# Kernel tuning notes

Hardware: AMD Instinct MI355X
Metric: run time of the kernel (lower is better)

Reference implementation:

```python
import jax, jax.numpy as jnp
import numpy as np

B, S, D = 2, 8192, 1024
H, HD, FD = 16, 64, 256

def setup_inputs() -> dict:
    key = jax.random.key(0)
    ks = jax.random.split(key, 6)
    sc = 1.0 / np.sqrt(D)
    return {
        "hidden_states": jax.random.normal(ks[0], (B, S, D), jnp.float32),
        "Wq": jax.random.normal(ks[1], (D, D), jnp.float32) * sc,
        "Wk": jax.random.normal(ks[2], (D, D), jnp.float32) * sc,
        "Wv": jax.random.normal(ks[3], (D, D), jnp.float32) * sc,
        "Wo": jax.random.normal(ks[4], (D, D), jnp.float32) * sc,
        "Wf": jax.random.normal(ks[5], (FD, HD), jnp.float32) * (1.0 / np.sqrt(HD)),
    }

def reference(hidden_states, Wq, Wk, Wv, Wo, Wf):
    b, s, _ = hidden_states.shape
    # projections (torch Linear: x @ W.T), split heads -> (b, s, h, hd)
    q = (hidden_states @ Wq.T).reshape(b, s, H, HD)
    k = (hidden_states @ Wk.T).reshape(b, s, H, HD)
    v = (hidden_states @ Wv.T).reshape(b, s, H, HD)
    # elu+1 feature map -> (b, s, h, f)
    qf = jax.nn.elu(q @ Wf.T) + 1.0
    kf = jax.nn.elu(k @ Wf.T) + 1.0
    # global kv summary: (b, h, f, d)
    kv = jnp.einsum('bshf,bshd->bhfd', kf, v)
    out = jnp.einsum('bshf,bhfd->bshd', qf, kv)
    k_sum = kf.sum(axis=1)                       # (b, h, f)
    norm = jnp.einsum('bshf,bhf->bsh', qf, k_sum)[..., None] + 1e-6
    out = (out / norm).reshape(b, s, D)
    return out @ Wo.T
```

## Files before the change

kernel.cpp:

```cpp
#include <hip/hip_runtime.h>
#include <stdint.h>

typedef __bf16 bf16_t;
typedef __attribute__((ext_vector_type(8))) __bf16 bfv8;
typedef __attribute__((ext_vector_type(4))) __bf16 bfv4;
typedef __attribute__((ext_vector_type(4))) float f32x4;

constexpr int BATCH = 2, SEQ = 8192, DIM = 1024, NH = 16, HDIM = 64, FDIM = 256;
constexpr int MROWS = BATCH * SEQ;
constexpr int NCHUNK = 16;
constexpr int KV_NIT = (SEQ / NCHUNK) / 32;
constexpr int KVP_CH = 32 * 256 * 68;

__device__ __forceinline__ f32x4 mfma_bf16(bfv8 a, bfv8 b, f32x4 c) {
  return __builtin_amdgcn_mfma_f32_16x16x32_bf16(a, b, c, 0, 0, 0);
}

__device__ __forceinline__ void gload_lds16(const bf16_t* g, bf16_t* lds) {
  auto const* gp = reinterpret_cast<const __attribute__((address_space(1))) uint32_t*>(
      reinterpret_cast<uintptr_t>(g));
  auto* lp = reinterpret_cast<__attribute__((address_space(3))) uint32_t*>(
      reinterpret_cast<uintptr_t>(lds));
  __builtin_amdgcn_global_load_lds(gp, lp, 16, 0, 0);
}

__device__ __forceinline__ void stage128x64(const bf16_t* g_base, int k0,
                                            bf16_t* lds, int wid, int lane) {
#pragma unroll
  for (int j = 0; j < 4; ++j) {
    int r0 = (wid * 4 + j) * 8;
    int g_row = r0 + (lane >> 3);
    int g_slot = (lane & 7) ^ (g_row & 7);
    const bf16_t* src = g_base + (size_t)g_row * DIM + k0 + g_slot * 8;
    gload_lds16(src, lds + r0 * 64);
  }
}

__global__ __launch_bounds__(256) void cvt_all(const float* __restrict__ X,
                                               const float* __restrict__ Wq,
                                               const float* __restrict__ Wk,
                                               const float* __restrict__ Wv,
                                               const float* __restrict__ Wo,
                                               const float* __restrict__ Wf,
                                               bf16_t* __restrict__ Xb,
                                               bf16_t* __restrict__ W3,
                                               bf16_t* __restrict__ Wob,
                                               bf16_t* __restrict__ Wfb) {
  int i = blockIdx.x * 256 + threadIdx.x;
  const float* src;
  bf16_t* dst;
  int off;
  if (i < 4194304) {
    src = X; dst = Xb; off = i;
  } else {
    int j = i - 4194304;
    if (j < 786432) {
      int seg = j >> 18;
      off = j & 262143;
      src = (seg == 0) ? Wq : ((seg == 1) ? Wk : Wv);
      dst = W3 + (size_t)seg * 1048576;
    } else if (j < 1048576) {
      off = j - 786432; src = Wo; dst = Wob;
    } else {
      off = j - 1048576; src = Wf; dst = Wfb;
    }
  }
  float4 v = reinterpret_cast<const float4*>(src)[off];
  bfv4 o = {(__bf16)v.x, (__bf16)v.y, (__bf16)v.z, (__bf16)v.w};
  reinterpret_cast<bfv4*>(dst)[off] = o;
}

__global__ __launch_bounds__(256) void gemm_qkv(const bf16_t* __restrict__ A,
                                                const bf16_t* __restrict__ Wall,
                                                bf16_t* __restrict__ Q,
                                                bf16_t* __restrict__ K,
                                                bf16_t* __restrict__ V) {
  __shared__ bf16_t As[2][128 * 64];
  __shared__ bf16_t Bs[2][128 * 64];
  int z = blockIdx.z;
  const bf16_t* Wm = Wall + (size_t)z * (DIM * DIM);
  bf16_t* C = (z == 0) ? Q : ((z == 1) ? K : V);
  int lane = threadIdx.x & 63, wid = threadIdx.x >> 6;
  int lr = lane & 15, lg = lane >> 4;
  int wr = wid >> 1, wc = wid & 1;
  int brow = blockIdx.x * 128, bcol = blockIdx.y * 128;
  const bf16_t* Ab = A + (size_t)brow * DIM;
  const bf16_t* Bb = Wm + (size_t)bcol * DIM;
  f32x4 acc[4][4] = {};

  stage128x64(Ab, 0, As[0], wid, lane);
  stage128x64(Bb, 0, Bs[0], wid, lane);
  asm volatile("s_waitcnt vmcnt(0)" ::: "memory");
  __builtin_amdgcn_s_barrier();

  auto TILE = [&](const bf16_t* Acur, const bf16_t* Bcur, bf16_t* Anext, bf16_t* Bnext,
                  int knext) __attribute__((always_inline)) {
    if (knext < DIM) {
      stage128x64(Ab, knext, Anext, wid, lane);
      stage128x64(Bb, knext, Bnext, wid, lane);
    }
#pragma unroll
    for (int kk = 0; kk < 2; ++kk) {
      bfv8 af[4], bg[4];
#pragma unroll
      for (int t = 0; t < 4; ++t) {
        int ar = wr * 64 + t * 16 + lr;
        af[t] = *reinterpret_cast<const bfv8*>(&Acur[ar * 64 + (((kk * 4 + lg) ^ (ar & 7)) * 8)]);
        int br = wc * 64 + t * 16 + lr;
        bg[t] = *reinterpret_cast<const bfv8*>(&Bcur[br * 64 + (((kk * 4 + lg) ^ (br & 7)) * 8)]);
      }
#pragma unroll
      for (int i = 0; i < 4; ++i)
#pragma unroll
        for (int j = 0; j < 4; ++j) acc[i][j] = mfma_bf16(af[i], bg[j], acc[i][j]);
    }
    asm volatile("s_waitcnt vmcnt(0)" ::: "memory");
    __builtin_amdgcn_s_barrier();
  };

  for (int ks = 0; ks < DIM / 64; ks += 2) {
    TILE(As[0], Bs[0], As[1], Bs[1], (ks + 1) * 64);
    TILE(As[1], Bs[1], As[0], Bs[0], (ks + 2) * 64);
  }

#pragma unroll
  for (int i = 0; i < 4; ++i) {
    int r = brow + wr * 64 + i * 16 + lg * 4;
#pragma unroll
    for (int j = 0; j < 4; ++j) {
      int c = bcol + wc * 64 + j * 16 + lr;
#pragma unroll
      for (int q = 0; q < 4; ++q) C[(size_t)(r + q) * DIM + c] = (__bf16)acc[i][j][q];
    }
  }
}

__global__ __launch_bounds__(256) void gemm_final(const bf16_t* __restrict__ A,
                                                  const bf16_t* __restrict__ W,
                                                  float* __restrict__ C) {
  __shared__ bf16_t As[2][128 * 64];
  __shared__ bf16_t Bs[2][128 * 64];
  int lane = threadIdx.x & 63, wid = threadIdx.x >> 6;
  int lr = lane & 15, lg = lane >> 4;
  int wr = wid >> 1, wc = wid & 1;
  int brow = blockIdx.x * 128, bcol = blockIdx.y * 128;
  const bf16_t* Ab = A + (size_t)brow * DIM;
  const bf16_t* Bb = W + (size_t)bcol * DIM;
  f32x4 acc[4][4] = {};

  stage128x64(Ab, 0, As[0], wid, lane);
  stage128x64(Bb, 0, Bs[0], wid, lane);
  asm volatile("s_waitcnt vmcnt(0)" ::: "memory");
  __builtin_amdgcn_s_barrier();

  auto TILE = [&](const bf16_t* Acur, const bf16_t* Bcur, bf16_t* Anext, bf16_t* Bnext,
                  int knext) __attribute__((always_inline)) {
    if (knext < DIM) {
      stage128x64(Ab, knext, Anext, wid, lane);
      stage128x64(Bb, knext, Bnext, wid, lane);
    }
#pragma unroll
    for (int kk = 0; kk < 2; ++kk) {
      bfv8 af[4], bg[4];
#pragma unroll
      for (int t = 0; t < 4; ++t) {
        int ar = wr * 64 + t * 16 + lr;
        af[t] = *reinterpret_cast<const bfv8*>(&Acur[ar * 64 + (((kk * 4 + lg) ^ (ar & 7)) * 8)]);
        int br = wc * 64 + t * 16 + lr;
        bg[t] = *reinterpret_cast<const bfv8*>(&Bcur[br * 64 + (((kk * 4 + lg) ^ (br & 7)) * 8)]);
      }
#pragma unroll
      for (int i = 0; i < 4; ++i)
#pragma unroll
        for (int j = 0; j < 4; ++j) acc[i][j] = mfma_bf16(af[i], bg[j], acc[i][j]);
    }
    asm volatile("s_waitcnt vmcnt(0)" ::: "memory");
    __builtin_amdgcn_s_barrier();
  };

  for (int ks = 0; ks < DIM / 64; ks += 2) {
    TILE(As[0], Bs[0], As[1], Bs[1], (ks + 1) * 64);
    TILE(As[1], Bs[1], As[0], Bs[0], (ks + 2) * 64);
  }

#pragma unroll
  for (int i = 0; i < 4; ++i) {
    int r = brow + wr * 64 + i * 16 + lg * 4;
#pragma unroll
    for (int j = 0; j < 4; ++j) {
      int c = bcol + wc * 64 + j * 16 + lr;
#pragma unroll
      for (int q = 0; q < 4; ++q) C[(size_t)(r + q) * DIM + c] = acc[i][j][q];
    }
  }
}

__global__ __launch_bounds__(256, 2) void kv_fused(const bf16_t* __restrict__ Kb,
                                                   const bf16_t* __restrict__ Vb,
                                                   const bf16_t* __restrict__ Wf,
                                                   float* __restrict__ kv_part) {
  __shared__ bf16_t vt[4][64 * 36];
  int chunk = blockIdx.x, bh = blockIdx.y;
  int b = bh >> 4, h = bh & 15;
  int lane = threadIdx.x & 63, wid = threadIdx.x >> 6;
  int lr = lane & 15, lg = lane >> 4;
  int f0 = wid * 64;
  bfv8 wf[4][2];
#pragma unroll
  for (int ft = 0; ft < 4; ++ft)
#pragma unroll
    for (int kk = 0; kk < 2; ++kk)
      wf[ft][kk] = *reinterpret_cast<const bfv8*>(Wf + (size_t)(f0 + ft * 16 + lr) * HDIM + kk * 32 + lg * 8);
  const bf16_t* Kbase = Kb + (size_t)b * SEQ * DIM + h * HDIM;
  const bf16_t* Vbase = Vb + (size_t)b * SEQ * DIM + h * HDIM;
  int s0 = chunk * (SEQ / NCHUNK);
  bfv8 ones;
#pragma unroll
  for (int j = 0; j < 8; ++j) ones[j] = (lr == 0) ? (__bf16)1.0f : (__bf16)0.0f;

  bfv8 krgA[2][2], krgB[2][2];
#pragma unroll
  for (int st = 0; st < 2; ++st)
#pragma unroll
    for (int kk = 0; kk < 2; ++kk)
      krgA[st][kk] = *reinterpret_cast<const bfv8*>(Kbase + (size_t)(s0 + st * 16 + lr) * DIM + kk * 32 + lg * 8);

  f32x4 acc[4][5] = {};

  auto STEP = [&](int it, bfv8(&krgC)[2][2], bfv8(&krgN)[2][2]) __attribute__((always_inline)) {
    int sb = s0 + it * 32;
    bfv8 vv[4];
#pragma unroll
    for (int rep = 0; rep < 4; ++rep) {
      int idx = rep * 64 + lane;
      vv[rep] = *reinterpret_cast<const bfv8*>(Vbase + (size_t)(sb + (idx >> 3)) * DIM + (idx & 7) * 8);
    }
    if (it + 1 < KV_NIT) {
#pragma unroll
      for (int st = 0; st < 2; ++st)
#pragma unroll
        for (int kk = 0; kk < 2; ++kk)
          krgN[st][kk] = *reinterpret_cast<const bfv8*>(Kbase + (size_t)(sb + 32 + st * 16 + lr) * DIM + kk * 32 + lg * 8);
    }
    f32x4 ckf[2][4] = {};
#pragma unroll
    for (int st = 0; st < 2; ++st)
#pragma unroll
      for (int ft = 0; ft < 4; ++ft)
#pragma unroll
        for (int kk = 0; kk < 2; ++kk) ckf[st][ft] = mfma_bf16(krgC[st][kk], wf[ft][kk], ckf[st][ft]);
#pragma unroll
    for (int rep = 0; rep < 4; ++rep) {
      int idx = rep * 64 + lane;
#pragma unroll
      for (int j = 0; j < 8; ++j) vt[wid][((idx & 7) * 8 + j) * 36 + (idx >> 3)] = vv[rep][j];
    }
    bfv8 af[4];
#pragma unroll
    for (int ft = 0; ft < 4; ++ft)
#pragma unroll
      for (int st = 0; st < 2; ++st)
#pragma unroll
        for (int q = 0; q < 4; ++q) {
          float x = ckf[st][ft][q];
          x = (x > 0.0f) ? (x + 1.0f) : __expf(x);
          af[ft][st * 4 + q] = (__bf16)x;
        }
    bfv8 bg[4];
#pragma unroll
    for (int nt = 0; nt < 4; ++nt) {
      bfv4 lo = *reinterpret_cast<const bfv4*>(&vt[wid][(nt * 16 + lr) * 36 + lg * 4]);
      bfv4 hi = *reinterpret_cast<const bfv4*>(&vt[wid][(nt * 16 + lr) * 36 + 16 + lg * 4]);
#pragma unroll
      for (int e = 0; e < 4; ++e) { bg[nt][e] = lo[e]; bg[nt][4 + e] = hi[e]; }
    }
#pragma unroll
    for (int ft = 0; ft < 4; ++ft) {
#pragma unroll
      for (int nt = 0; nt < 4; ++nt) acc[ft][nt] = mfma_bf16(af[ft], bg[nt], acc[ft][nt]);
      acc[ft][4] = mfma_bf16(af[ft], ones, acc[ft][4]);
    }
  };

  for (int it2 = 0; it2 < KV_NIT; it2 += 2) {
    STEP(it2, krgA, krgB);
    STEP(it2 + 1, krgB, krgA);
  }

  float* outb = kv_part + ((size_t)chunk * 32 + bh) * (FDIM * 68);
#pragma unroll
  for (int ft = 0; ft < 4; ++ft)
#pragma unroll
    for (int q = 0; q < 4; ++q) {
      int f = f0 + ft * 16 + lg * 4 + q;
#pragma unroll
      for (int nt = 0; nt < 4; ++nt)
        outb[(size_t)f * 68 + nt * 16 + lr] = acc[ft][nt][q];
      if (lr < 4) outb[(size_t)f * 68 + 64 + lr] = acc[ft][4][q];
    }
}

__global__ __launch_bounds__(256) void kv_reduce(const float* __restrict__ part,
                                                 bf16_t* __restrict__ kvT) {
  int i = blockIdx.x * 256 + threadIdx.x;
  if (i < KVP_CH) {
    int n = i % 68;
    int t = i / 68;
    int f = t & 255, bh = t >> 8;
    float s = 0.0f;
#pragma unroll
    for (int c = 0; c < NCHUNK; ++c) s += part[(size_t)c * KVP_CH + i];
    int fs = ((((f >> 3) ^ (n & 7)) << 3) | (f & 7));
    kvT[((size_t)bh * 80 + n) * FDIM + fs] = (__bf16)s;
  } else {
    int j = i - KVP_CH;
    int f = j & 255;
    int t = j >> 8;
    int n = 68 + t % 12, bh = t / 12;
    kvT[((size_t)bh * 80 + n) * FDIM + f] = (__bf16)0.0f;
  }
}

__global__ __launch_bounds__(256) void attn_fused(const bf16_t* __restrict__ Qb,
                                                  const bf16_t* __restrict__ Wf,
                                                  const bf16_t* __restrict__ kvT,
                                                  bf16_t* __restrict__ outp) {
  __shared__ bf16_t qf_lds[64 * 264];
  __shared__ bf16_t kv_lds[80 * 256];
  int rb = blockIdx.x, h = blockIdx.y;
  int row0 = rb * 64;
  int bh = (row0 >> 13) * NH + h;
  int lane = threadIdx.x & 63, wid = threadIdx.x >> 6;
  int lr = lane & 15, lg = lane >> 4;
  int f0 = wid * 64;
  const bf16_t* kvTb = kvT + (size_t)bh * 80 * FDIM;
#pragma unroll
  for (int i = 0; i < 10; ++i) {
    int sbase = wid * 640 + i * 64;
    gload_lds16(kvTb + (size_t)(sbase + lane) * 8, kv_lds + sbase * 8);
  }
  bfv8 qa[4][2], wfb[4][2];
#pragma unroll
  for (int t = 0; t < 4; ++t)
#pragma unroll
    for (int kk = 0; kk < 2; ++kk) {
      qa[t][kk] = *reinterpret_cast<const bfv8*>(Qb + (size_t)(row0 + t * 16 + lr) * DIM + h * HDIM + kk * 32 + lg * 8);
      wfb[t][kk] = *reinterpret_cast<const bfv8*>(Wf + (size_t)(f0 + t * 16 + lr) * HDIM + kk * 32 + lg * 8);
    }
  f32x4 cq[4][4] = {};
#pragma unroll
  for (int rt = 0; rt < 4; ++rt)
#pragma unroll
    for (int ft = 0; ft < 4; ++ft)
#pragma unroll
      for (int kk = 0; kk < 2; ++kk) cq[rt][ft] = mfma_bf16(qa[rt][kk], wfb[ft][kk], cq[rt][ft]);
#pragma unroll
  for (int rt = 0; rt < 4; ++rt)
#pragma unroll
    for (int ft = 0; ft < 4; ++ft)
#pragma unroll
      for (int q = 0; q < 4; ++q) {
        float x = cq[rt][ft][q];
        x = (x > 0.0f) ? (x + 1.0f) : __expf(x);
        qf_lds[(size_t)(rt * 16 + lg * 4 + q) * 264 + f0 + ft * 16 + lr] = (__bf16)x;
      }
  __syncthreads();
  f32x4 acc[5] = {};
#pragma unroll
  for (int ks = 0; ks < 8; ++ks) {
    bfv8 a = *reinterpret_cast<const bfv8*>(&qf_lds[(size_t)(wid * 16 + lr) * 264 + ks * 32 + lg * 8]);
#pragma unroll
    for (int nt = 0; nt < 5; ++nt) {
      bfv8 bg = *reinterpret_cast<const bfv8*>(
          &kv_lds[(size_t)(nt * 16 + lr) * 256 + (((ks * 4 + lg) ^ (lr & 7)) * 8)]);
      acc[nt] = mfma_bf16(a, bg, acc[nt]);
    }
  }
  __syncthreads();
#pragma unroll
  for (int q = 0; q < 4; ++q) {
    float nrm = __shfl(acc[4][q], (lane & 48)) + 1e-6f;
    int row = wid * 16 + lg * 4 + q;
#pragma unroll
    for (int nt = 0; nt < 4; ++nt)
      qf_lds[(size_t)row * 264 + nt * 16 + lr] = (__bf16)(acc[nt][q] / nrm);
  }
  __syncthreads();
#pragma unroll
  for (int rep = 0; rep < 2; ++rep) {
    int id = rep * 256 + threadIdx.x;
    int row = id >> 3, c8 = id & 7;
    bfv8 v = *reinterpret_cast<const bfv8*>(&qf_lds[(size_t)row * 264 + c8 * 8]);
    *reinterpret_cast<bfv8*>(&outp[(size_t)(row0 + row) * DIM + h * HDIM + c8 * 8]) = v;
  }
}

extern "C" void kernel_launch(void* const* d_in, const int* in_sizes, int n_in,
                              void* d_out, int out_size, void* d_ws, size_t ws_size,
                              hipStream_t stream) {
  const float* X  = (const float*)d_in[0];
  const float* Wq = (const float*)d_in[1];
  const float* Wk = (const float*)d_in[2];
  const float* Wv = (const float*)d_in[3];
  const float* Wo = (const float*)d_in[4];
  const float* Wf = (const float*)d_in[5];
  float* out = (float*)d_out;
  char* ws = (char*)d_ws;
  const size_t MB = 1ull << 20;
  if (ws_size < 75 * MB) return;

  bf16_t* Xb  = (bf16_t*)(ws + 0 * MB);
  bf16_t* W3  = (bf16_t*)(ws + 32 * MB);
  bf16_t* Qb  = (bf16_t*)(ws + 38 * MB);
  bf16_t* Wob = (bf16_t*)(ws + 70 * MB);
  bf16_t* Wfb = (bf16_t*)(ws + 72 * MB);
  bf16_t* kvT = (bf16_t*)(ws + 73 * MB);
  float* kv_part = (float*)(ws + 0 * MB);
  bf16_t* outp = (bf16_t*)(ws + 0 * MB);
  bf16_t* Kb = (bf16_t*)d_out;
  bf16_t* Vb = Kb + (size_t)MROWS * DIM;

  cvt_all<<<20496, 256, 0, stream>>>(X, Wq, Wk, Wv, Wo, Wf, Xb, W3, Wob, Wfb);

  gemm_qkv<<<dim3(128, 8, 3), 256, 0, stream>>>(Xb, W3, Qb, Kb, Vb);
  kv_fused<<<dim3(NCHUNK, 32), 256, 0, stream>>>(Kb, Vb, Wfb, kv_part);
  kv_reduce<<<2560, 256, 0, stream>>>(kv_part, kvT);
  attn_fused<<<dim3(256, NH), 256, 0, stream>>>(Qb, Wfb, kvT, outp);
  gemm_final<<<dim3(128, 8), 256, 0, stream>>>(outp, Wob, out);
}
```

Before: 282.6 us.

## Deepen GEMM pipeline to four-stage K32 ring with partial vmcnt waits

Both projection GEMMs switch from a double-buffered K=64 tile loop with full vmcnt(0) waits to a four-buffer ring of K=32 tiles, keeping three stages of global-to-LDS loads in flight and waiting with vmcnt(8). The LDS swizzle changes to a rotation scheme that fits 32-wide rows. The goal is to hide global load latency behind MFMA work instead of draining the memory queue every tile. In exchange there are twice as many barriers per K, and the result depends on the hand-counted vmcnt values matching the number of outstanding loads.

```diff
diff --git a/kernel.cpp b/kernel.cpp
--- a/kernel.cpp
+++ b/kernel.cpp
@@ -24,15 +24,15 @@
   __builtin_amdgcn_global_load_lds(gp, lp, 16, 0, 0);
 }
 
-__device__ __forceinline__ void stage128x64(const bf16_t* g_base, int k0,
+__device__ __forceinline__ void stage128x32(const bf16_t* g_base, int k0,
                                             bf16_t* lds, int wid, int lane) {
 #pragma unroll
-  for (int j = 0; j < 4; ++j) {
-    int r0 = (wid * 4 + j) * 8;
-    int g_row = r0 + (lane >> 3);
-    int g_slot = (lane & 7) ^ (g_row & 7);
+  for (int j = 0; j < 2; ++j) {
+    int r0 = (wid * 2 + j) * 16;
+    int g_row = r0 + (lane >> 2);
+    int g_slot = ((lane & 3) - ((g_row >> 1) & 3)) & 3;
     const bf16_t* src = g_base + (size_t)g_row * DIM + k0 + g_slot * 8;
-    gload_lds16(src, lds + r0 * 64);
+    gload_lds16(src, lds + r0 * 32);
   }
 }
 
@@ -70,13 +70,18 @@
   reinterpret_cast<bfv4*>(dst)[off] = o;
 }
 
+#define VM8() asm volatile("s_waitcnt vmcnt(8)" ::: "memory")
+#define VM4() asm volatile("s_waitcnt vmcnt(4)" ::: "memory")
+#define VM0() asm volatile("s_waitcnt vmcnt(0)" ::: "memory")
+#define BAR() __builtin_amdgcn_s_barrier()
+
 __global__ __launch_bounds__(256) void gemm_qkv(const bf16_t* __restrict__ A,
                                                 const bf16_t* __restrict__ Wall,
                                                 bf16_t* __restrict__ Q,
                                                 bf16_t* __restrict__ K,
                                                 bf16_t* __restrict__ V) {
-  __shared__ bf16_t As[2][128 * 64];
-  __shared__ bf16_t Bs[2][128 * 64];
+  __shared__ bf16_t As[4][128 * 32];
+  __shared__ bf16_t Bs[4][128 * 32];
   int z = blockIdx.z;
   const bf16_t* Wm = Wall + (size_t)z * (DIM * DIM);
   bf16_t* C = (z == 0) ? Q : ((z == 1) ? K : V);
@@ -88,40 +93,37 @@
   const bf16_t* Bb = Wm + (size_t)bcol * DIM;
   f32x4 acc[4][4] = {};
 
-  stage128x64(Ab, 0, As[0], wid, lane);
-  stage128x64(Bb, 0, Bs[0], wid, lane);
-  asm volatile("s_waitcnt vmcnt(0)" ::: "memory");
-  __builtin_amdgcn_s_barrier();
-
-  auto TILE = [&](const bf16_t* Acur, const bf16_t* Bcur, bf16_t* Anext, bf16_t* Bnext,
-                  int knext) __attribute__((always_inline)) {
-    if (knext < DIM) {
-      stage128x64(Ab, knext, Anext, wid, lane);
-      stage128x64(Bb, knext, Bnext, wid, lane);
-    }
-#pragma unroll
-    for (int kk = 0; kk < 2; ++kk) {
-      bfv8 af[4], bg[4];
-#pragma unroll
-      for (int t = 0; t < 4; ++t) {
-        int ar = wr * 64 + t * 16 + lr;
-        af[t] = *reinterpret_cast<const bfv8*>(&Acur[ar * 64 + (((kk * 4 + lg) ^ (ar & 7)) * 8)]);
-        int br = wc * 64 + t * 16 + lr;
-        bg[t] = *reinterpret_cast<const bfv8*>(&Bcur[br * 64 + (((kk * 4 + lg) ^ (br & 7)) * 8)]);
-      }
-#pragma unroll
-      for (int i = 0; i < 4; ++i)
-#pragma unroll
-        for (int j = 0; j < 4; ++j) acc[i][j] = mfma_bf16(af[i], bg[j], acc[i][j]);
-    }
-    asm volatile("s_waitcnt vmcnt(0)" ::: "memory");
-    __builtin_amdgcn_s_barrier();
+  auto STAGE = [&](int t, int buf) __attribute__((always_inline)) {
+    stage128x32(Ab, t * 32, As[buf], wid, lane);
+    stage128x32(Bb, t * 32, Bs[buf], wid, lane);
   };
-
-  for (int ks = 0; ks < DIM / 64; ks += 2) {
-    TILE(As[0], Bs[0], As[1], Bs[1], (ks + 1) * 64);
-    TILE(As[1], Bs[1], As[0], Bs[0], (ks + 2) * 64);
-  }
+  auto COMPUTE = [&](const bf16_t* Acur, const bf16_t* Bcur) __attribute__((always_inline)) {
+    bfv8 af[4], bg[4];
+#pragma unroll
+    for (int t = 0; t < 4; ++t) {
+      int ar = wr * 64 + t * 16 + lr;
+      af[t] = *reinterpret_cast<const bfv8*>(&Acur[ar * 32 + (((lg + (ar >> 1)) & 3) * 8)]);
+      int br = wc * 64 + t * 16 + lr;
+      bg[t] = *reinterpret_cast<const bfv8*>(&Bcur[br * 32 + (((lg + (br >> 1)) & 3) * 8)]);
+    }
+#pragma unroll
+    for (int i = 0; i < 4; ++i)
+#pragma unroll
+      for (int j = 0; j < 4; ++j) acc[i][j] = mfma_bf16(af[i], bg[j], acc[i][j]);
+  };
+
+  STAGE(0, 0); STAGE(1, 1); STAGE(2, 2);
+  for (int I = 0; I < 7; ++I) {
+    int t0 = I * 4;
+    VM8(); BAR(); STAGE(t0 + 3, 3); COMPUTE(As[0], Bs[0]);
+    VM8(); BAR(); STAGE(t0 + 4, 0); COMPUTE(As[1], Bs[1]);
+    VM8(); BAR(); STAGE(t0 + 5, 1); COMPUTE(As[2], Bs[2]);
+    VM8(); BAR(); STAGE(t0 + 6, 2); COMPUTE(As[3], Bs[3]);
+  }
+  VM8(); BAR(); STAGE(31, 3); COMPUTE(As[0], Bs[0]);
+  VM8(); BAR(); COMPUTE(As[1], Bs[1]);
+  VM4(); BAR(); COMPUTE(As[2], Bs[2]);
+  VM0(); BAR(); COMPUTE(As[3], Bs[3]);
 
 #pragma unroll
   for (int i = 0; i < 4; ++i) {
@@ -138,8 +140,8 @@
 __global__ __launch_bounds__(256) void gemm_final(const bf16_t* __restrict__ A,
                                                   const bf16_t* __restrict__ W,
                                                   float* __restrict__ C) {
-  __shared__ bf16_t As[2][128 * 64];
-  __shared__ bf16_t Bs[2][128 * 64];
+  __shared__ bf16_t As[4][128 * 32];
+  __shared__ bf16_t Bs[4][128 * 32];
   int lane = threadIdx.x & 63, wid = threadIdx.x >> 6;
   int lr = lane & 15, lg = lane >> 4;
   int wr = wid >> 1, wc = wid & 1;
@@ -148,40 +150,37 @@
   const bf16_t* Bb = W + (size_t)bcol * DIM;
   f32x4 acc[4][4] = {};
 
-  stage128x64(Ab, 0, As[0], wid, lane);
-  stage128x64(Bb, 0, Bs[0], wid, lane);
-  asm volatile("s_waitcnt vmcnt(0)" ::: "memory");
-  __builtin_amdgcn_s_barrier();
-
-  auto TILE = [&](const bf16_t* Acur, const bf16_t* Bcur, bf16_t* Anext, bf16_t* Bnext,
-                  int knext) __attribute__((always_inline)) {
-    if (knext < DIM) {
-      stage128x64(Ab, knext, Anext, wid, lane);
-      stage128x64(Bb, knext, Bnext, wid, lane);
-    }
-#pragma unroll
-    for (int kk = 0; kk < 2; ++kk) {
-      bfv8 af[4], bg[4];
-#pragma unroll
-      for (int t = 0; t < 4; ++t) {
-        int ar = wr * 64 + t * 16 + lr;
-        af[t] = *reinterpret_cast<const bfv8*>(&Acur[ar * 64 + (((kk * 4 + lg) ^ (ar & 7)) * 8)]);
-        int br = wc * 64 + t * 16 + lr;
-        bg[t] = *reinterpret_cast<const bfv8*>(&Bcur[br * 64 + (((kk * 4 + lg) ^ (br & 7)) * 8)]);
-      }
-#pragma unroll
-      for (int i = 0; i < 4; ++i)
-#pragma unroll
-        for (int j = 0; j < 4; ++j) acc[i][j] = mfma_bf16(af[i], bg[j], acc[i][j]);
-    }
-    asm volatile("s_waitcnt vmcnt(0)" ::: "memory");
-    __builtin_amdgcn_s_barrier();
+  auto STAGE = [&](int t, int buf) __attribute__((always_inline)) {
+    stage128x32(Ab, t * 32, As[buf], wid, lane);
+    stage128x32(Bb, t * 32, Bs[buf], wid, lane);
   };
-
-  for (int ks = 0; ks < DIM / 64; ks += 2) {
-    TILE(As[0], Bs[0], As[1], Bs[1], (ks + 1) * 64);
-    TILE(As[1], Bs[1], As[0], Bs[0], (ks + 2) * 64);
-  }
+  auto COMPUTE = [&](const bf16_t* Acur, const bf16_t* Bcur) __attribute__((always_inline)) {
+    bfv8 af[4], bg[4];
+#pragma unroll
+    for (int t = 0; t < 4; ++t) {
+      int ar = wr * 64 + t * 16 + lr;
+      af[t] = *reinterpret_cast<const bfv8*>(&Acur[ar * 32 + (((lg + (ar >> 1)) & 3) * 8)]);
+      int br = wc * 64 + t * 16 + lr;
+      bg[t] = *reinterpret_cast<const bfv8*>(&Bcur[br * 32 + (((lg + (br >> 1)) & 3) * 8)]);
+    }
+#pragma unroll
+    for (int i = 0; i < 4; ++i)
+#pragma unroll
+      for (int j = 0; j < 4; ++j) acc[i][j] = mfma_bf16(af[i], bg[j], acc[i][j]);
+  };
+
+  STAGE(0, 0); STAGE(1, 1); STAGE(2, 2);
+  for (int I = 0; I < 7; ++I) {
+    int t0 = I * 4;
+    VM8(); BAR(); STAGE(t0 + 3, 3); COMPUTE(As[0], Bs[0]);
+    VM8(); BAR(); STAGE(t0 + 4, 0); COMPUTE(As[1], Bs[1]);
+    VM8(); BAR(); STAGE(t0 + 5, 1); COMPUTE(As[2], Bs[2]);
+    VM8(); BAR(); STAGE(t0 + 6, 2); COMPUTE(As[3], Bs[3]);
+  }
+  VM8(); BAR(); STAGE(31, 3); COMPUTE(As[0], Bs[0]);
+  VM8(); BAR(); COMPUTE(As[1], Bs[1]);
+  VM4(); BAR(); COMPUTE(As[2], Bs[2]);
+  VM0(); BAR(); COMPUTE(As[3], Bs[3]);
 
 #pragma unroll
   for (int i = 0; i < 4; ++i) {
@@ -194,6 +193,11 @@
     }
   }
 }
+
+#undef VM8
+#undef VM4
+#undef VM0
+#undef BAR
 
 __global__ __launch_bounds__(256, 2) void kv_fused(const bf16_t* __restrict__ Kb,
                                                    const bf16_t* __restrict__ Vb,
```

Result: slower. 309.9 us (+9.6%).
